# Kernel optimization log

Hardware: AMD Instinct MI355X
Metric: run time of the kernel (lower is better)

## Reference

```python
import jax, jax.numpy as jnp
import numpy as np

N_HEADS = 16  # cfg.n_heads
ROPE_BASE = 10000.0


def _rope_sin_cos(T, head_dim, dtype):
    # standard NeoX-style rotary tables, shape (T, head_dim)
    inv_freq = 1.0 / (ROPE_BASE ** (jnp.arange(0, head_dim, 2, dtype=jnp.float32) / head_dim))
    freqs = jnp.arange(T, dtype=jnp.float32)[:, None] * inv_freq[None, :]  # (T, hd/2)
    emb = jnp.concatenate([freqs, freqs], axis=-1)                          # (T, hd)
    return jnp.sin(emb).astype(dtype), jnp.cos(emb).astype(dtype)


def _rotate_half(x):
    x1, x2 = jnp.split(x, 2, axis=-1)
    return jnp.concatenate([-x2, x1], axis=-1)


def setup_inputs() -> dict:
    key = jax.random.key(0)
    kx, kq, kp, kl = jax.random.split(key, 4)
    B, T, D = 4, 2048, 2048
    x = jax.random.normal(kx, (B, T, D), dtype=jnp.float32)
    # torch Linear weights: (out_features, in_features), no bias
    Wqkv = jax.random.normal(kq, (3 * D, D), dtype=jnp.float32) * (D ** -0.5)
    Wproj = jax.random.normal(kp, (D, D), dtype=jnp.float32) * (D ** -0.5)
    # padding at the end: valid lengths in [T//2, T]
    lengths = jax.random.randint(kl, (B,), T // 2, T + 1)
    attention_mask = (jnp.arange(T)[None, :] < lengths[:, None]).astype(jnp.int32)
    return {"x": x, "Wqkv": Wqkv, "Wproj": Wproj, "attention_mask": attention_mask}


def reference(x, Wqkv, Wproj, attention_mask):
    B, T, D = x.shape
    H = N_HEADS
    hd = D // H
    qkv = (x @ Wqkv.T).reshape(B, T, 3, H, hd)            # (B,T,3,H,hd)
    q, k, v = (jnp.moveaxis(qkv[:, :, i], 1, 2) for i in range(3))  # each (B,H,T,hd)
    sin, cos = _rope_sin_cos(T, hd, x.dtype)              # (T,hd), broadcast over B,H
    q = q * cos + _rotate_half(q) * sin
    k = k * cos + _rotate_half(k) * sin
    scale = 1.0 / jnp.sqrt(jnp.asarray(hd, x.dtype))
    scores = jnp.einsum("bhqd,bhkd->bhqk", q, k) * scale  # (B,H,T,T)
    causal = jnp.triu(jnp.ones((T, T), dtype=bool), k=1)[None, None]       # (1,1,T,T)
    pad = (attention_mask == 0)[:, None, None, :]                           # (B,1,1,T)
    bias = jnp.where(causal | pad, -jnp.inf, 0.0).astype(x.dtype)
    attn = jax.nn.softmax(scores + bias, axis=-1)
    out = jnp.einsum("bhqk,bhkd->bhqd", attn, v)          # (B,H,T,hd)
    out = jnp.moveaxis(out, 1, 2).reshape(B, T, D)
    return out @ Wproj.T
```

## Files before the change

### kernel.cpp

```cpp
#include <hip/hip_runtime.h>
#include <math.h>

#define B_SZ 4
#define T_SEQ 2048
#define D_MODEL 2048
#define NH 16
#define HD 128

typedef unsigned short u16;
typedef unsigned int u32;
typedef __attribute__((ext_vector_type(8))) short short8;
typedef __attribute__((ext_vector_type(4))) float f32x4;

__device__ __forceinline__ float bf2f(u16 u) {
    return __uint_as_float(((u32)u) << 16);
}
__device__ __forceinline__ u16 f2bf(float f) {
    u32 x = __float_as_uint(f);
    return (u16)((x + 0x7fffu + ((x >> 16) & 1u)) >> 16);
}

__device__ __forceinline__ void gload_lds16(const u16* g, u16* lds) {
    __builtin_amdgcn_global_load_lds(
        (const __attribute__((address_space(1))) u32*)(const void*)g,
        (__attribute__((address_space(3))) u32*)(void*)lds, 16, 0, 0);
}

__global__ __launch_bounds__(256) void cast_kernel(const float* __restrict__ in,
                                                   u16* __restrict__ out, int n4)
{
    int idx = blockIdx.x * 256 + threadIdx.x;
    if (idx < n4) {
        float4 x = ((const float4*)in)[idx];
        ushort4 u;
        u.x = f2bf(x.x); u.y = f2bf(x.y); u.z = f2bf(x.z); u.w = f2bf(x.w);
        ((ushort4*)out)[idx] = u;
    }
}

#define TSZ 16384
#define MFMA_B16 __builtin_amdgcn_mfma_f32_16x16x32_bf16

template <int MODE>
__global__ __launch_bounds__(512, 2) void gemm256(
    const u16* __restrict__ A, const u16* __restrict__ W,
    float* __restrict__ C,
    u16* __restrict__ qb, u16* __restrict__ kb, u16* __restrict__ vb,
    int M, int N, int K)
{
    extern __shared__ u16 smem[];

    const int tid = threadIdx.x;
    const int nbx = N >> 8;
    const int nwg = gridDim.x;
    const int orig = blockIdx.x;
    const int wgid = (orig & 7) * (nwg >> 3) + (orig >> 3);
    const int bx = wgid % nbx, by = wgid / nbx;
    const int n0 = bx << 8, m0 = by << 8;

    const int w = tid >> 6, L = tid & 63;
    const int wm = w >> 2, wn = w & 3;
    const int lr = L & 15;
    const int lqb = (L >> 4) << 4;
    const int xorv = (lr & 7) << 4;
    const int cb0 = lqb ^ xorv;
    const int cb1 = (64 + lqb) ^ xorv;

    const u16* Ag = A + (size_t)m0 * K;
    const u16* Wg = W + (size_t)n0 * K;

    const int srow = tid >> 3;
    const int scb = ((tid << 4) & 127) ^ ((srow & 7) << 4);
    const size_t goff = (size_t)srow * K + (scb >> 1);
    const int loff = tid << 3;

    const int NT = K >> 6;

    f32x4 acc[8][4];
#pragma unroll
    for (int i = 0; i < 8; ++i)
#pragma unroll
        for (int j = 0; j < 4; ++j) acc[i][j] = (f32x4){0.f, 0.f, 0.f, 0.f};

#define ST_A(tt, c) gload_lds16(Ag + (size_t)((c) * 64) * K + (size_t)(tt) * 64 + goff, \
                                smem + ((tt) & 1) * TSZ + (c) * 4096 + loff)
#define ST_B(tt, c) gload_lds16(Wg + (size_t)((c) * 64) * K + (size_t)(tt) * 64 + goff, \
                                smem + 2 * TSZ + ((tt) & 1) * TSZ + (c) * 4096 + loff)

    ST_A(0, 0); ST_A(0, 2); ST_B(0, 0); ST_B(0, 1); ST_B(0, 2); ST_B(0, 3);
    ST_A(0, 1); ST_A(0, 3);
    ST_A(1, 0); ST_A(1, 2); ST_B(1, 0); ST_B(1, 1); ST_B(1, 2); ST_B(1, 3);
    asm volatile("s_waitcnt vmcnt(6)" ::: "memory");
    __builtin_amdgcn_s_barrier();

    for (int t = 0; t < NT; ++t) {
        const char* pA = (const char*)(smem + (t & 1) * TSZ) + (wm * 128 + lr) * 128;
        const char* pB = (const char*)(smem + 2 * TSZ + (t & 1) * TSZ) + (wn * 64 + lr) * 128;
        short8 alo[4][2], ahi[4][2], blo[2][2], bhi[2][2];

#pragma unroll
        for (int f = 0; f < 4; ++f) {
            alo[f][0] = *(const short8*)(pA + f * 2048 + cb0);
            alo[f][1] = *(const short8*)(pA + f * 2048 + cb1);
        }
#pragma unroll
        for (int g = 0; g < 2; ++g) {
            blo[g][0] = *(const short8*)(pB + g * 2048 + cb0);
            blo[g][1] = *(const short8*)(pB + g * 2048 + cb1);
        }
        if (t + 1 < NT) { ST_A(t + 1, 1); ST_A(t + 1, 3); }
        asm volatile("s_waitcnt lgkmcnt(8)" ::: "memory");
        __builtin_amdgcn_s_barrier();
        asm volatile("s_waitcnt lgkmcnt(0)" ::: "memory");
        __builtin_amdgcn_sched_barrier(0);
        __builtin_amdgcn_s_setprio(1);
#pragma unroll
        for (int f = 0; f < 4; ++f)
#pragma unroll
            for (int g = 0; g < 2; ++g) {
                acc[f][g] = MFMA_B16(alo[f][0], blo[g][0], acc[f][g], 0, 0, 0);
                acc[f][g] = MFMA_B16(alo[f][1], blo[g][1], acc[f][g], 0, 0, 0);
            }
        __builtin_amdgcn_s_setprio(0);
        __builtin_amdgcn_s_barrier();

#pragma unroll
        for (int g = 0; g < 2; ++g) {
            bhi[g][0] = *(const short8*)(pB + 4096 + g * 2048 + cb0);
            bhi[g][1] = *(const short8*)(pB + 4096 + g * 2048 + cb1);
        }
        if (t + 2 < NT) { ST_A(t + 2, 0); ST_A(t + 2, 2); }
        __builtin_amdgcn_s_barrier();
        asm volatile("s_waitcnt lgkmcnt(0)" ::: "memory");
        __builtin_amdgcn_sched_barrier(0);
        __builtin_amdgcn_s_setprio(1);
#pragma unroll
        for (int f = 0; f < 4; ++f)
#pragma unroll
            for (int g = 0; g < 2; ++g) {
                acc[f][2 + g] = MFMA_B16(alo[f][0], bhi[g][0], acc[f][2 + g], 0, 0, 0);
                acc[f][2 + g] = MFMA_B16(alo[f][1], bhi[g][1], acc[f][2 + g], 0, 0, 0);
            }
        __builtin_amdgcn_s_setprio(0);
        __builtin_amdgcn_s_barrier();

#pragma unroll
        for (int f = 0; f < 4; ++f) {
            ahi[f][0] = *(const short8*)(pA + 8192 + f * 2048 + cb0);
            ahi[f][1] = *(const short8*)(pA + 8192 + f * 2048 + cb1);
        }
        if (t + 2 < NT) { ST_B(t + 2, 0); ST_B(t + 2, 1); }
        __builtin_amdgcn_s_barrier();
        asm volatile("s_waitcnt lgkmcnt(0)" ::: "memory");
        __builtin_amdgcn_sched_barrier(0);
        __builtin_amdgcn_s_setprio(1);
#pragma unroll
        for (int f = 0; f < 4; ++f)
#pragma unroll
            for (int g = 0; g < 2; ++g) {
                acc[4 + f][g] = MFMA_B16(ahi[f][0], blo[g][0], acc[4 + f][g], 0, 0, 0);
                acc[4 + f][g] = MFMA_B16(ahi[f][1], blo[g][1], acc[4 + f][g], 0, 0, 0);
            }
        __builtin_amdgcn_s_setprio(0);
        __builtin_amdgcn_s_barrier();

        if (t + 2 < NT) { ST_B(t + 2, 2); ST_B(t + 2, 3); }
        if (t < NT - 2)
            asm volatile("s_waitcnt vmcnt(6)" ::: "memory");
        else
            asm volatile("s_waitcnt vmcnt(0)" ::: "memory");
        __builtin_amdgcn_s_barrier();
        __builtin_amdgcn_s_setprio(1);
#pragma unroll
        for (int f = 0; f < 4; ++f)
#pragma unroll
            for (int g = 0; g < 2; ++g) {
                acc[4 + f][2 + g] = MFMA_B16(ahi[f][0], bhi[g][0], acc[4 + f][2 + g], 0, 0, 0);
                acc[4 + f][2 + g] = MFMA_B16(ahi[f][1], bhi[g][1], acc[4 + f][2 + g], 0, 0, 0);
            }
        __builtin_amdgcn_s_setprio(0);
        __builtin_amdgcn_s_barrier();
    }
#undef ST_A
#undef ST_B

    const int lq4 = (L >> 4) << 2;

    if (MODE == 0) {
#pragma unroll
        for (int f = 0; f < 8; ++f) {
            const int m = m0 + wm * 128 + (f >> 2) * 64 + (f & 3) * 16 + lq4;
#pragma unroll
            for (int g = 0; g < 4; ++g) {
                const int n = n0 + wn * 64 + (g >> 1) * 32 + (g & 1) * 16 + lr;
#pragma unroll
                for (int r = 0; r < 4; ++r)
                    C[(size_t)(m + r) * N + n] = acc[f][g][r];
            }
        }
    } else {
        const int s = n0 >> 11;
        const int b_ = m0 >> 11;
        const int t0 = m0 & (T_SEQ - 1);
        if (s == 2) {
            u16* Ts = smem;
#pragma unroll
            for (int f = 0; f < 8; ++f) {
                const int tl = wm * 128 + (f >> 2) * 64 + (f & 3) * 16 + lq4;
#pragma unroll
                for (int g = 0; g < 4; ++g) {
                    const int c = wn * 64 + (g >> 1) * 32 + (g & 1) * 16 + lr;
                    char* rowp = (char*)Ts + c * 512;
#pragma unroll
                    for (int r = 0; r < 4; ++r)
                        *(u16*)(rowp + (((tl + r) * 2) ^ ((c & 7) << 4))) =
                            f2bf(acc[f][g][r]);
                }
            }
            __syncthreads();
            const int h0 = (n0 & 2047) >> 7;
            const int tcb = (tid & 31) << 4;
#pragma unroll
            for (int pass = 0; pass < 16; ++pass) {
                const int c = pass * 16 + (tid >> 5);
                short8 vv = *(const short8*)((const char*)Ts + c * 512 +
                                             (tcb ^ ((c & 7) << 4)));
                const int hh = c >> 7, d = c & 127;
                *(short8*)(vb + ((size_t)(b_ * NH + h0 + hh) * HD + d) * T_SEQ +
                           t0 + (tcb >> 1)) = vv;
            }
        } else {
            u16* p = (s == 0) ? qb : kb;
            const int nb = n0 & 2047;
#pragma unroll
            for (int f = 0; f < 8; ++f) {
                const int tl = t0 + wm * 128 + (f >> 2) * 64 + (f & 3) * 16 + lq4;
#pragma unroll
                for (int g = 0; g < 4; ++g) {
                    const int nn = nb + wn * 64 + (g >> 1) * 32 + (g & 1) * 16 + lr;
                    const int hh = nn >> 7, d = nn & 127;
                    u16* pb = p + ((size_t)(b_ * NH + hh) * T_SEQ + tl) * HD + d;
#pragma unroll
                    for (int r = 0; r < 4; ++r)
                        pb[(size_t)r * HD] = f2bf(acc[f][g][r]);
                }
            }
        }
    }
}

__global__ __launch_bounds__(128) void rope_kernel(u16* __restrict__ qb,
                                                   u16* __restrict__ kb)
{
    const int bht = blockIdx.x;
    const int t = bht & (T_SEQ - 1);
    const int bh = bht >> 11;
    const int tid = threadIdx.x;
    const int i = tid & 63;
    u16* buf = (tid < 64) ? qb : kb;
    const size_t base = ((size_t)bh * T_SEQ + t) * HD;

    const float inv = expf(-(2.f * (float)i / 128.f) * 9.210340371976184f);
    const float ang = (float)t * inv;
    const float s = sinf(ang);
    const float c = cosf(ang);

    const float x1 = bf2f(buf[base + i]);
    const float x2 = bf2f(buf[base + i + 64]);
    buf[base + i]      = f2bf(x1 * c - x2 * s);
    buf[base + i + 64] = f2bf(x2 * c + x1 * s);
}

__device__ __forceinline__ void stage_k64(const u16* g, u16* lds, int tid) {
#pragma unroll
    for (int c = 0; c < 4; ++c) {
        const int row = c * 16 + (tid >> 4);
        const int cb = ((tid & 15) * 16) ^ ((row & 7) << 4);
        gload_lds16(g + (size_t)row * HD + (cb >> 1), lds + c * 2048 + tid * 8);
    }
}
__device__ __forceinline__ void stage_v64(const u16* g, u16* lds, int tid) {
#pragma unroll
    for (int c = 0; c < 4; ++c) {
        const int row = c * 32 + (tid >> 3);
        const int cb = ((tid & 7) * 16) ^ ((row & 7) << 4);
        gload_lds16(g + (size_t)row * T_SEQ + (cb >> 1), lds + c * 2048 + tid * 8);
    }
}

__global__ __launch_bounds__(256) void attn_kernel(
    const u16* __restrict__ q, const u16* __restrict__ k,
    const u16* __restrict__ v, const int* __restrict__ mask,
    u16* __restrict__ o)
{
    extern __shared__ u16 smem[];
    u16* Kb = smem;
    u16* Vb = smem + 16384;

    const int tid = threadIdx.x;
    const int id = blockIdx.x;
    const int bh = id >> 5;
    const int qi = 31 - (id & 31);
    const int b = bh >> 4;
    const int q0 = qi * 64;
    const int w = tid >> 6, L = tid & 63;
    const int lr = L & 15;
    const int lqB = (L >> 4) * 16;
    const int xk = (lr & 7) << 4;
    const float scale = 0.08838834764831845f;
    const float NEG = -1e30f;

    char* PsW = (char*)(smem + 32768 + w * 1024);

    const u16* qg = q + (size_t)bh * T_SEQ * HD;
    const u16* kg = k + (size_t)bh * T_SEQ * HD;
    const u16* vg = v + (size_t)bh * HD * T_SEQ;
    const int* mrow = mask + b * T_SEQ;

    stage_k64(qg + (size_t)q0 * HD, Kb, tid);

    int4 ma = ((const int4*)mrow)[tid];
    int4 mb2 = ((const int4*)mrow)[tid + 256];
    int part = ma.x + ma.y + ma.z + ma.w + mb2.x + mb2.y + mb2.z + mb2.w;
#pragma unroll
    for (int off = 32; off >= 1; off >>= 1) part += __shfl_xor(part, off);
    int* lred = (int*)(smem + 32768);
    if (L == 0) lred[w] = part;
    __syncthreads();
    const int len = lred[0] + lred[1] + lred[2] + lred[3];

    short8 qa[4];
    {
        const char* Kc = (const char*)Kb;
        const int row = w * 16 + lr;
#pragma unroll
        for (int kc = 0; kc < 4; ++kc)
            qa[kc] = *(const short8*)(Kc + row * 256 + ((kc * 64 + lqB) ^ xk));
    }
    __syncthreads();

    stage_k64(kg, Kb, tid);
    stage_v64(vg, Vb, tid);

    f32x4 on[8];
#pragma unroll
    for (int nd = 0; nd < 8; ++nd) on[nd] = (f32x4){0.f, 0.f, 0.f, 0.f};
    float l_r[4] = {0.f, 0.f, 0.f, 0.f};
    const int row_base = q0 + w * 16 + (L >> 4) * 4;

    for (int kt = 0; kt <= qi; ++kt) {
        const int kv0 = kt * 64;
        const int cur = kt & 1;
        if (kt < qi) {
            stage_k64(kg + (size_t)(kv0 + 64) * HD, Kb + (cur ^ 1) * 8192, tid);
            stage_v64(vg + (kv0 + 64), Vb + (cur ^ 1) * 8192, tid);
            asm volatile("s_waitcnt vmcnt(8)" ::: "memory");
        } else {
            asm volatile("s_waitcnt vmcnt(0)" ::: "memory");
        }
        __builtin_amdgcn_s_barrier();

        const char* Kc = (const char*)(Kb + cur * 8192);
        const char* Vc = (const char*)(Vb + cur * 8192);

        f32x4 sacc[4];
        short8 bb[4][4];
#pragma unroll
        for (int nt = 0; nt < 4; ++nt) {
            const char* rp = Kc + (nt * 16 + lr) * 256;
#pragma unroll
            for (int kc = 0; kc < 4; ++kc)
                bb[nt][kc] = *(const short8*)(rp + ((kc * 64 + lqB) ^ xk));
        }
        __builtin_amdgcn_s_setprio(1);
#pragma unroll
        for (int nt = 0; nt < 4; ++nt) {
            sacc[nt] = (f32x4){0.f, 0.f, 0.f, 0.f};
#pragma unroll
            for (int kc = 0; kc < 4; ++kc)
                sacc[nt] = MFMA_B16(qa[kc], bb[nt][kc], sacc[nt], 0, 0, 0);
        }
        __builtin_amdgcn_s_setprio(0);

        const bool diag = (kt == qi);
        float ps_[4][4];
#pragma unroll
        for (int nt = 0; nt < 4; ++nt) {
            const int col = kv0 + nt * 16 + lr;
            const float bias = (col < len) ? 0.f : NEG;
#pragma unroll
            for (int r = 0; r < 4; ++r) {
                float s = sacc[nt][r] * scale + bias;
                if (diag && col > row_base + r) s = NEG;
                const float p = __expf(s);
                ps_[nt][r] = p;
                l_r[r] += p;
            }
        }

#pragma unroll
        for (int nt = 0; nt < 4; ++nt) {
#pragma unroll
            for (int r = 0; r < 4; ++r) {
                const int pr = (L >> 4) * 4 + r;
                *(u16*)(PsW + pr * 128 + (((nt * 16 + lr) * 2) ^ ((pr & 7) << 4))) =
                    f2bf(ps_[nt][r]);
            }
        }

        short8 pa0 = *(const short8*)(PsW + lr * 128 + (lqB ^ xk));
        short8 pa1 = *(const short8*)(PsW + lr * 128 + ((64 + lqB) ^ xk));
        __builtin_amdgcn_s_setprio(1);
#pragma unroll
        for (int nd = 0; nd < 8; ++nd) {
            const char* vp = Vc + (nd * 16 + lr) * 128;
            short8 vb0 = *(const short8*)(vp + (lqB ^ xk));
            short8 vb1 = *(const short8*)(vp + ((64 + lqB) ^ xk));
            on[nd] = MFMA_B16(pa0, vb0, on[nd], 0, 0, 0);
            on[nd] = MFMA_B16(pa1, vb1, on[nd], 0, 0, 0);
        }
        __builtin_amdgcn_s_setprio(0);
        __builtin_amdgcn_s_barrier();
    }

#pragma unroll
    for (int off = 1; off < 16; off <<= 1)
#pragma unroll
        for (int r = 0; r < 4; ++r)
            l_r[r] += __shfl_xor(l_r[r], off);

    const int h = bh & 15;
#pragma unroll
    for (int r = 0; r < 4; ++r) {
        const float inv = 1.f / l_r[r];
        const int t = row_base + r;
        u16* op = o + ((size_t)(b * T_SEQ + t)) * D_MODEL + h * HD + lr;
#pragma unroll
        for (int nd = 0; nd < 8; ++nd)
            op[nd * 16] = f2bf(on[nd][r] * inv);
    }
}

extern "C" void kernel_launch(void* const* d_in, const int* in_sizes, int n_in,
                              void* d_out, int out_size, void* d_ws, size_t ws_size,
                              hipStream_t stream)
{
    const float* x     = (const float*)d_in[0];
    const float* Wqkv  = (const float*)d_in[1];
    const float* Wproj = (const float*)d_in[2];
    const int*   mask  = (const int*)d_in[3];
    float* out = (float*)d_out;

    const size_t E = (size_t)B_SZ * T_SEQ * D_MODEL;
    u16* xb     = (u16*)d_ws;
    u16* wqkvb  = xb + E;
    u16* wprojb = wqkvb + (size_t)3 * D_MODEL * D_MODEL;
    u16* qb     = wprojb + (size_t)D_MODEL * D_MODEL;
    u16* kb     = qb + E;
    u16* vb     = kb + E;
    u16* ob     = vb + E;

    const int M = B_SZ * T_SEQ;

    cast_kernel<<<dim3((int)(E / 4 / 256)), 256, 0, stream>>>(x, xb, (int)(E / 4));
    cast_kernel<<<dim3(3 * D_MODEL * D_MODEL / 4 / 256), 256, 0, stream>>>(
        Wqkv, wqkvb, 3 * D_MODEL * D_MODEL / 4);
    cast_kernel<<<dim3(D_MODEL * D_MODEL / 4 / 256), 256, 0, stream>>>(
        Wproj, wprojb, D_MODEL * D_MODEL / 4);

    gemm256<1><<<dim3((3 * D_MODEL / 256) * (M / 256)), 512, 131072, stream>>>(
        xb, wqkvb, nullptr, qb, kb, vb, M, 3 * D_MODEL, D_MODEL);

    rope_kernel<<<dim3(B_SZ * NH * T_SEQ), 128, 0, stream>>>(qb, kb);

    attn_kernel<<<dim3(T_SEQ / 64 * 64), 256, 73728, stream>>>(qb, kb, vb, mask, ob);

    gemm256<0><<<dim3((D_MODEL / 256) * (M / 256)), 512, 131072, stream>>>(
        ob, wprojb, out, nullptr, nullptr, nullptr, M, D_MODEL, D_MODEL);
}
```

Before: 661.2 us.

## Use 128-row query tiles with 8 waves and register-staged V in attention

```diff
diff --git a/kernel.cpp b/kernel.cpp
--- a/kernel.cpp
+++ b/kernel.cpp
@@ -271,38 +271,30 @@
     buf[base + i + 64] = f2bf(x2 * c + x1 * s);
 }
 
-__device__ __forceinline__ void stage_k64(const u16* g, u16* lds, int tid) {
-#pragma unroll
-    for (int c = 0; c < 4; ++c) {
-        const int row = c * 16 + (tid >> 4);
+__device__ __forceinline__ void stage_k_512(const u16* g, u16* lds, int tid) {
+#pragma unroll
+    for (int c = 0; c < 2; ++c) {
+        const int row = c * 32 + (tid >> 4);
         const int cb = ((tid & 15) * 16) ^ ((row & 7) << 4);
-        gload_lds16(g + (size_t)row * HD + (cb >> 1), lds + c * 2048 + tid * 8);
-    }
-}
-__device__ __forceinline__ void stage_v64(const u16* g, u16* lds, int tid) {
-#pragma unroll
-    for (int c = 0; c < 4; ++c) {
-        const int row = c * 32 + (tid >> 3);
-        const int cb = ((tid & 7) * 16) ^ ((row & 7) << 4);
-        gload_lds16(g + (size_t)row * T_SEQ + (cb >> 1), lds + c * 2048 + tid * 8);
-    }
-}
-
-__global__ __launch_bounds__(256) void attn_kernel(
+        gload_lds16(g + (size_t)row * HD + (cb >> 1), lds + c * 4096 + tid * 8);
+    }
+}
+
+__global__ __launch_bounds__(512, 4) void attn_kernel(
     const u16* __restrict__ q, const u16* __restrict__ k,
     const u16* __restrict__ v, const int* __restrict__ mask,
     u16* __restrict__ o)
 {
     extern __shared__ u16 smem[];
     u16* Kb = smem;
-    u16* Vb = smem + 16384;
+    char* Vs = (char*)smem + 32768;
 
     const int tid = threadIdx.x;
     const int id = blockIdx.x;
-    const int bh = id >> 5;
-    const int qi = 31 - (id & 31);
+    const int bh = id & 63;
+    const int qi = 15 - (id >> 6);
     const int b = bh >> 4;
-    const int q0 = qi * 64;
+    const int q0 = qi * 128;
     const int w = tid >> 6, L = tid & 63;
     const int lr = L & 15;
     const int lqB = (L >> 4) * 16;
@@ -310,117 +302,142 @@
     const float scale = 0.08838834764831845f;
     const float NEG = -1e30f;
 
-    char* PsW = (char*)(smem + 32768 + w * 1024);
+    char* PsW = (char*)smem + 49152 + w * 2048;
 
     const u16* qg = q + (size_t)bh * T_SEQ * HD;
     const u16* kg = k + (size_t)bh * T_SEQ * HD;
     const u16* vg = v + (size_t)bh * HD * T_SEQ;
     const int* mrow = mask + b * T_SEQ;
 
-    stage_k64(qg + (size_t)q0 * HD, Kb, tid);
-
-    int4 ma = ((const int4*)mrow)[tid];
-    int4 mb2 = ((const int4*)mrow)[tid + 256];
-    int part = ma.x + ma.y + ma.z + ma.w + mb2.x + mb2.y + mb2.z + mb2.w;
+#pragma unroll
+    for (int c = 0; c < 4; ++c) {
+        const int row = c * 32 + (tid >> 4);
+        const int cb = ((tid & 15) * 16) ^ ((row & 7) << 4);
+        gload_lds16(qg + (size_t)(q0 + row) * HD + (cb >> 1),
+                    smem + c * 4096 + tid * 8);
+    }
+    int4 m4 = ((const int4*)mrow)[tid];
+    int part = m4.x + m4.y + m4.z + m4.w;
 #pragma unroll
     for (int off = 32; off >= 1; off >>= 1) part += __shfl_xor(part, off);
-    int* lred = (int*)(smem + 32768);
+    int* lred = (int*)((char*)smem + 49152);
     if (L == 0) lred[w] = part;
     __syncthreads();
-    const int len = lred[0] + lred[1] + lred[2] + lred[3];
+    int len = 0;
+#pragma unroll
+    for (int i = 0; i < 8; ++i) len += lred[i];
 
     short8 qa[4];
     {
-        const char* Kc = (const char*)Kb;
+        const char* Qc = (const char*)smem;
         const int row = w * 16 + lr;
 #pragma unroll
         for (int kc = 0; kc < 4; ++kc)
-            qa[kc] = *(const short8*)(Kc + row * 256 + ((kc * 64 + lqB) ^ xk));
+            qa[kc] = *(const short8*)(Qc + row * 256 + ((kc * 64 + lqB) ^ xk));
     }
     __syncthreads();
 
-    stage_k64(kg, Kb, tid);
-    stage_v64(vg, Vb, tid);
+    const int lim = 2 * qi + 1;
+
+    stage_k_512(kg, Kb, tid);
+    const int vr0 = tid >> 3, vr1 = 64 + (tid >> 3);
+    const int vce = (tid & 7) * 8;
+    const int vcb = (tid & 7) * 16;
+    short8 vc0 = *(const short8*)(vg + (size_t)vr0 * T_SEQ + vce);
+    short8 vc1 = *(const short8*)(vg + (size_t)vr1 * T_SEQ + vce);
+    short8 vn0 = vc0, vn1 = vc1;
 
     f32x4 on[8];
 #pragma unroll
     for (int nd = 0; nd < 8; ++nd) on[nd] = (f32x4){0.f, 0.f, 0.f, 0.f};
     float l_r[4] = {0.f, 0.f, 0.f, 0.f};
-    const int row_base = q0 + w * 16 + (L >> 4) * 4;
-
-    for (int kt = 0; kt <= qi; ++kt) {
+    const int wrow0 = q0 + w * 16;
+    const int row_base = wrow0 + (L >> 4) * 4;
+
+    for (int kt = 0; kt <= lim; ++kt) {
         const int kv0 = kt * 64;
         const int cur = kt & 1;
-        if (kt < qi) {
-            stage_k64(kg + (size_t)(kv0 + 64) * HD, Kb + (cur ^ 1) * 8192, tid);
-            stage_v64(vg + (kv0 + 64), Vb + (cur ^ 1) * 8192, tid);
-            asm volatile("s_waitcnt vmcnt(8)" ::: "memory");
+        if (kt < lim) {
+            stage_k_512(kg + (size_t)(kv0 + 64) * HD, Kb + (cur ^ 1) * 8192, tid);
+            vn0 = *(const short8*)(vg + (size_t)vr0 * T_SEQ + (kv0 + 64) + vce);
+            vn1 = *(const short8*)(vg + (size_t)vr1 * T_SEQ + (kv0 + 64) + vce);
+            asm volatile("s_waitcnt vmcnt(4)" ::: "memory");
         } else {
             asm volatile("s_waitcnt vmcnt(0)" ::: "memory");
         }
         __builtin_amdgcn_s_barrier();
 
-        const char* Kc = (const char*)(Kb + cur * 8192);
-        const char* Vc = (const char*)(Vb + cur * 8192);
-
-        f32x4 sacc[4];
-        short8 bb[4][4];
-#pragma unroll
-        for (int nt = 0; nt < 4; ++nt) {
-            const char* rp = Kc + (nt * 16 + lr) * 256;
-#pragma unroll
-            for (int kc = 0; kc < 4; ++kc)
-                bb[nt][kc] = *(const short8*)(rp + ((kc * 64 + lqB) ^ xk));
-        }
-        __builtin_amdgcn_s_setprio(1);
-#pragma unroll
-        for (int nt = 0; nt < 4; ++nt) {
-            sacc[nt] = (f32x4){0.f, 0.f, 0.f, 0.f};
-#pragma unroll
-            for (int kc = 0; kc < 4; ++kc)
-                sacc[nt] = MFMA_B16(qa[kc], bb[nt][kc], sacc[nt], 0, 0, 0);
-        }
-        __builtin_amdgcn_s_setprio(0);
-
-        const bool diag = (kt == qi);
+        *(short8*)(Vs + vr0 * 128 + (vcb ^ ((vr0 & 7) << 4))) = vc0;
+        *(short8*)(Vs + vr1 * 128 + (vcb ^ ((vr1 & 7) << 4))) = vc1;
+
+        const bool active = (kv0 <= wrow0 + 15);
         float ps_[4][4];
-#pragma unroll
-        for (int nt = 0; nt < 4; ++nt) {
-            const int col = kv0 + nt * 16 + lr;
-            const float bias = (col < len) ? 0.f : NEG;
-#pragma unroll
-            for (int r = 0; r < 4; ++r) {
-                float s = sacc[nt][r] * scale + bias;
-                if (diag && col > row_base + r) s = NEG;
-                const float p = __expf(s);
-                ps_[nt][r] = p;
-                l_r[r] += p;
-            }
-        }
-
-#pragma unroll
-        for (int nt = 0; nt < 4; ++nt) {
-#pragma unroll
-            for (int r = 0; r < 4; ++r) {
-                const int pr = (L >> 4) * 4 + r;
-                *(u16*)(PsW + pr * 128 + (((nt * 16 + lr) * 2) ^ ((pr & 7) << 4))) =
-                    f2bf(ps_[nt][r]);
-            }
-        }
-
-        short8 pa0 = *(const short8*)(PsW + lr * 128 + (lqB ^ xk));
-        short8 pa1 = *(const short8*)(PsW + lr * 128 + ((64 + lqB) ^ xk));
-        __builtin_amdgcn_s_setprio(1);
-#pragma unroll
-        for (int nd = 0; nd < 8; ++nd) {
-            const char* vp = Vc + (nd * 16 + lr) * 128;
-            short8 vb0 = *(const short8*)(vp + (lqB ^ xk));
-            short8 vb1 = *(const short8*)(vp + ((64 + lqB) ^ xk));
-            on[nd] = MFMA_B16(pa0, vb0, on[nd], 0, 0, 0);
-            on[nd] = MFMA_B16(pa1, vb1, on[nd], 0, 0, 0);
-        }
-        __builtin_amdgcn_s_setprio(0);
-        __builtin_amdgcn_s_barrier();
+        if (active) {
+            const char* Kc = (const char*)(Kb + cur * 8192);
+            f32x4 sacc[4];
+            short8 bb[4][4];
+#pragma unroll
+            for (int nt = 0; nt < 4; ++nt) {
+                const char* rp = Kc + (nt * 16 + lr) * 256;
+#pragma unroll
+                for (int kc = 0; kc < 4; ++kc)
+                    bb[nt][kc] = *(const short8*)(rp + ((kc * 64 + lqB) ^ xk));
+            }
+            __builtin_amdgcn_s_setprio(1);
+#pragma unroll
+            for (int nt = 0; nt < 4; ++nt) {
+                sacc[nt] = (f32x4){0.f, 0.f, 0.f, 0.f};
+#pragma unroll
+                for (int kc = 0; kc < 4; ++kc)
+                    sacc[nt] = MFMA_B16(qa[kc], bb[nt][kc], sacc[nt], 0, 0, 0);
+            }
+            __builtin_amdgcn_s_setprio(0);
+
+            const bool diag = (kv0 + 63 > wrow0);
+#pragma unroll
+            for (int nt = 0; nt < 4; ++nt) {
+                const int col = kv0 + nt * 16 + lr;
+                const float bias = (col < len) ? 0.f : NEG;
+#pragma unroll
+                for (int r = 0; r < 4; ++r) {
+                    float s = sacc[nt][r] * scale + bias;
+                    if (diag && col > row_base + r) s = NEG;
+                    const float p = __expf(s);
+                    ps_[nt][r] = p;
+                    l_r[r] += p;
+                }
+            }
+        }
+
+        asm volatile("s_waitcnt lgkmcnt(0)" ::: "memory");
+        __builtin_amdgcn_s_barrier();
+
+        if (active) {
+#pragma unroll
+            for (int nt = 0; nt < 4; ++nt) {
+#pragma unroll
+                for (int r = 0; r < 4; ++r) {
+                    const int pr = (L >> 4) * 4 + r;
+                    *(u16*)(PsW + pr * 128 +
+                            (((nt * 16 + lr) * 2) ^ ((pr & 7) << 4))) =
+                        f2bf(ps_[nt][r]);
+                }
+            }
+
+            short8 pa0 = *(const short8*)(PsW + lr * 128 + (lqB ^ xk));
+            short8 pa1 = *(const short8*)(PsW + lr * 128 + ((64 + lqB) ^ xk));
+            __builtin_amdgcn_s_setprio(1);
+#pragma unroll
+            for (int nd = 0; nd < 8; ++nd) {
+                const char* vp = Vs + (nd * 16 + lr) * 128;
+                short8 vb0 = *(const short8*)(vp + (lqB ^ xk));
+                short8 vb1 = *(const short8*)(vp + ((64 + lqB) ^ xk));
+                on[nd] = MFMA_B16(pa0, vb0, on[nd], 0, 0, 0);
+                on[nd] = MFMA_B16(pa1, vb1, on[nd], 0, 0, 0);
+            }
+            __builtin_amdgcn_s_setprio(0);
+        }
+        vc0 = vn0; vc1 = vn1;
     }
 
 #pragma unroll
@@ -473,7 +490,7 @@
 
     rope_kernel<<<dim3(B_SZ * NH * T_SEQ), 128, 0, stream>>>(qb, kb);
 
-    attn_kernel<<<dim3(T_SEQ / 64 * 64), 256, 73728, stream>>>(qb, kb, vb, mask, ob);
+    attn_kernel<<<dim3(16 * 64), 512, 65536, stream>>>(qb, kb, vb, mask, ob);
 
     gemm256<0><<<dim3((D_MODEL / 256) * (M / 256)), 512, 131072, stream>>>(
         ob, wprojb, out, nullptr, nullptr, nullptr, M, D_MODEL, D_MODEL);
```

Measured after the change: 787.8 us. 19.1% more time.
